# Kernel tuning notes

Hardware: AMD Instinct MI355X
Metric: run time of the kernel (lower is better)

## Reference

```python
import jax, jax.numpy as jnp
import numpy as np

B, S, MODEL_DIM = 4, 512, 128
FEAT = 2 * MODEL_DIM  # hidden feature dim must be 2*model_dim for Ws


def setup_inputs() -> dict:
    key = jax.random.key(0)
    k1, k2, k3 = jax.random.split(key, 3)
    hidden = jax.random.normal(k1, (B, S, FEAT), dtype=jnp.float32)
    # nn.Linear(2*model_dim, model_dim, bias=False): weight [model_dim, 2*model_dim]
    Ws = jax.random.normal(k2, (MODEL_DIM, FEAT), dtype=jnp.float32) * (1.0 / np.sqrt(FEAT))
    # nn.Linear(model_dim, 1, bias=False): weight [1, model_dim]
    vs = jax.random.normal(k3, (1, MODEL_DIM), dtype=jnp.float32) * (1.0 / np.sqrt(MODEL_DIM))
    return {"hidden": hidden, "Ws": Ws, "vs": vs}


def reference(hidden, Ws, vs):
    # query*key broadcast: [B, S, S, 2D]
    prod = hidden[:, None, :, :] * hidden[:, :, None, :]
    # MLP score: Linear -> tanh -> Linear, squeeze -> [B, S, S]
    h = jnp.tanh(jnp.einsum('bqkf,df->bqkd', prod, Ws))
    sjt = jnp.einsum('bqkd,d->bqk', h, vs[0])
    atten = jax.nn.softmax(sjt, axis=2)  # dropout = identity (eval)
    context = jnp.einsum('bqk,bkf->bqf', atten, hidden)
    return (context, atten)
```

## Files before the change

kernel.cpp:

```cpp
#include <hip/hip_runtime.h>
#include <hip/hip_bf16.h>

#define Bb 4
#define Ss 512
#define Ff 256
#define Dd 128

typedef __attribute__((ext_vector_type(8))) short bf8_t;
typedef __attribute__((ext_vector_type(4))) float f32x4;

__device__ __forceinline__ short bfbits(float x) {
  union { __hip_bfloat16 b; short s; } u;
  u.b = __hip_bfloat16(x);
  return u.s;
}

__device__ __forceinline__ float fast_tanh(float x) {
  float e = exp2f(x * 2.8853900818f);
  return 1.0f - 2.0f * __builtin_amdgcn_rcpf(e + 1.0f);
}

typedef __attribute__((address_space(3))) unsigned int lds_u32;
typedef const __attribute__((address_space(1))) unsigned int glb_u32;
__device__ __forceinline__ void load_lds16(const void* g, void* l) {
  __builtin_amdgcn_global_load_lds((glb_u32*)g, (lds_u32*)l, 16, 0, 0);
}

__global__ __launch_bounds__(256) void cvt_kernel(const float* __restrict__ hidden,
                                                  short* __restrict__ hbf) {
  const int idx = blockIdx.x * 256 + threadIdx.x;
  const int lin = idx * 4;
  const float4 v = *(const float4*)(hidden + lin);
  const int r = lin >> 8;
  const int c = lin & 255;
  const int cs = c ^ ((r & 7) << 3);
  short4 o = make_short4(bfbits(v.x), bfbits(v.y), bfbits(v.z), bfbits(v.w));
  *(short4*)(hbf + ((size_t)r << 8) + cs) = o;
}

__global__ __launch_bounds__(256) void score_kernel(
    const float* __restrict__ hidden, const short* __restrict__ hbf,
    const float* __restrict__ Ws, const float* __restrict__ vs,
    float* __restrict__ Sws)
{
  __shared__ __align__(16) short htile[2][32 * 256];
  __shared__ float s_full[2][512];

  const int tid   = threadIdx.x;
  const int lane  = tid & 63;
  const int w     = tid >> 6;
  const int col16 = lane & 15;
  const int grp   = lane >> 4;

  const int blk  = blockIdx.x;
  const int b    = blk & 3;
  const int pair = blk >> 2;
  const int q0   = pair * 2;
  const int c0   = q0 >> 5;

  const float* Hb  = hidden + (size_t)b * Ss * Ff;
  const short* hsb = hbf + (size_t)b * Ss * Ff;
  float*       Sb  = Sws + (size_t)b * Ss * Ss;

  bf8_t afr[2][2][8];
  #pragma unroll
  for (int ks = 0; ks < 8; ++ks) {
    const int f0 = ks * 32 + grp * 8;
    float4 h0[2], h1[2];
    #pragma unroll
    for (int g = 0; g < 2; ++g) {
      const float* hq = Hb + (size_t)(q0 + g) * Ff + f0;
      h0[g] = *(const float4*)(hq);
      h1[g] = *(const float4*)(hq + 4);
    }
    #pragma unroll
    for (int mf = 0; mf < 2; ++mf) {
      const int d = w * 32 + mf * 16 + col16;
      const float* wr = Ws + (size_t)d * Ff + f0;
      const float4 w0 = *(const float4*)(wr);
      const float4 w1 = *(const float4*)(wr + 4);
      #pragma unroll
      for (int g = 0; g < 2; ++g) {
        bf8_t t;
        t[0] = bfbits(h0[g].x * w0.x); t[1] = bfbits(h0[g].y * w0.y);
        t[2] = bfbits(h0[g].z * w0.z); t[3] = bfbits(h0[g].w * w0.w);
        t[4] = bfbits(h1[g].x * w1.x); t[5] = bfbits(h1[g].y * w1.y);
        t[6] = bfbits(h1[g].z * w1.z); t[7] = bfbits(h1[g].w * w1.w);
        afr[g][mf][ks] = t;
      }
    }
  }

  float vsv[2][4];
  #pragma unroll
  for (int mf = 0; mf < 2; ++mf)
    #pragma unroll
    for (int r = 0; r < 4; ++r)
      vsv[mf][r] = vs[w * 32 + mf * 16 + grp * 4 + r];

  {
    float* sf = (float*)s_full;
    #pragma unroll
    for (int i = 0; i < 4; ++i) sf[i * 256 + tid] = 0.f;
  }

  {
    const short* src = hsb + c0 * (32 * 256);
    #pragma unroll
    for (int i = 0; i < 4; ++i) {
      const int seg = i * 4 + w;
      load_lds16(src + seg * 512 + lane * 8, &htile[0][seg * 512]);
    }
  }

  const int swz = (col16 & 7) << 3;

  int cur = 0;
  for (int c = c0; c < 16; ++c) {
    const int k0 = c << 5;
    __syncthreads();
    if (c < 15) {
      const short* src = hsb + (c + 1) * (32 * 256);
      const int nb = cur ^ 1;
      #pragma unroll
      for (int i = 0; i < 4; ++i) {
        const int seg = i * 4 + w;
        load_lds16(src + seg * 512 + lane * 8, &htile[nb][seg * 512]);
      }
    }
    #pragma unroll
    for (int nf = 0; nf < 2; ++nf) {
      f32x4 acc[2][2] = {};
      const int rbase = nf * 4096 + col16 * 256;
      #pragma unroll
      for (int ks = 0; ks < 8; ++ks) {
        const int coff = (ks * 32 + grp * 8) ^ swz;
        const bf8_t bbv = *(const bf8_t*)(&htile[cur][rbase + coff]);
        acc[0][0] = __builtin_amdgcn_mfma_f32_16x16x32_bf16(afr[0][0][ks], bbv, acc[0][0], 0, 0, 0);
        acc[0][1] = __builtin_amdgcn_mfma_f32_16x16x32_bf16(afr[0][1][ks], bbv, acc[0][1], 0, 0, 0);
        acc[1][0] = __builtin_amdgcn_mfma_f32_16x16x32_bf16(afr[1][0][ks], bbv, acc[1][0], 0, 0, 0);
        acc[1][1] = __builtin_amdgcn_mfma_f32_16x16x32_bf16(afr[1][1][ks], bbv, acc[1][1], 0, 0, 0);
      }
      #pragma unroll
      for (int g = 0; g < 2; ++g) {
        float ps = 0.f;
        #pragma unroll
        for (int mf = 0; mf < 2; ++mf)
          #pragma unroll
          for (int r = 0; r < 4; ++r)
            ps += vsv[mf][r] * fast_tanh(acc[g][mf][r]);
        ps += __shfl_xor(ps, 16);
        ps += __shfl_xor(ps, 32);
        if (lane < 16)
          atomicAdd(&s_full[g][k0 + nf * 16 + lane], ps);
      }
    }
    cur ^= 1;
  }
  __syncthreads();

  #pragma unroll
  for (int g = 0; g < 2; ++g) {
    for (int k = q0 + tid; k < Ss; k += 256)
      Sb[(size_t)(q0 + g) * Ss + k] = s_full[g][k];
    for (int k = q0 + 2 + tid; k < Ss; k += 256)
      Sb[(size_t)k * Ss + (q0 + g)] = s_full[g][k];
  }
}

__global__ __launch_bounds__(256) void ctx_kernel(
    const float* __restrict__ hidden, const float* __restrict__ Sws,
    float* __restrict__ out)
{
  __shared__ float p[4][512];
  __shared__ float ctxp[4][4][256];

  const int tid = threadIdx.x, lane = tid & 63, w = tid >> 6;
  const int blk = blockIdx.x;
  const int b   = blk >> 7;
  const int q0  = (blk & 127) * 4;

  const float* Sb = Sws + (size_t)b * Ss * Ss;
  const float* Hb = hidden + (size_t)b * Ss * Ff;

  {
    const int q = q0 + w;
    const float* Srow = Sb + (size_t)q * Ss;
    const float4 x0 = *(const float4*)(Srow + lane * 8);
    const float4 x1 = *(const float4*)(Srow + lane * 8 + 4);
    float m = fmaxf(fmaxf(fmaxf(x0.x, x0.y), fmaxf(x0.z, x0.w)),
                    fmaxf(fmaxf(x1.x, x1.y), fmaxf(x1.z, x1.w)));
    #pragma unroll
    for (int d = 1; d < 64; d <<= 1) m = fmaxf(m, __shfl_xor(m, d));
    float4 e0, e1;
    e0.x = exp2f((x0.x - m) * 1.44269504f); e0.y = exp2f((x0.y - m) * 1.44269504f);
    e0.z = exp2f((x0.z - m) * 1.44269504f); e0.w = exp2f((x0.w - m) * 1.44269504f);
    e1.x = exp2f((x1.x - m) * 1.44269504f); e1.y = exp2f((x1.y - m) * 1.44269504f);
    e1.z = exp2f((x1.z - m) * 1.44269504f); e1.w = exp2f((x1.w - m) * 1.44269504f);
    float sm = e0.x + e0.y + e0.z + e0.w + e1.x + e1.y + e1.z + e1.w;
    #pragma unroll
    for (int d = 1; d < 64; d <<= 1) sm += __shfl_xor(sm, d);
    const float inv = 1.0f / sm;
    e0.x *= inv; e0.y *= inv; e0.z *= inv; e0.w *= inv;
    e1.x *= inv; e1.y *= inv; e1.z *= inv; e1.w *= inv;
    float* att = out + (size_t)Bb * Ss * Ff + ((size_t)(b * Ss + q)) * Ss;
    *(float4*)(att + lane * 8)     = e0;
    *(float4*)(att + lane * 8 + 4) = e1;
    *(float4*)(&p[w][lane * 8])     = e0;
    *(float4*)(&p[w][lane * 8 + 4]) = e1;
  }
  __syncthreads();

  float4 cg[4] = {{0,0,0,0},{0,0,0,0},{0,0,0,0},{0,0,0,0}};
  const float* hp = Hb + (size_t)(w * 128) * Ff + lane * 4;
  #pragma unroll 4
  for (int k = 0; k < 128; ++k) {
    const float4 h = *(const float4*)(hp + (size_t)k * Ff);
    #pragma unroll
    for (int g = 0; g < 4; ++g) {
      const float a = p[g][w * 128 + k];
      cg[g].x += a * h.x; cg[g].y += a * h.y; cg[g].z += a * h.z; cg[g].w += a * h.w;
    }
  }
  #pragma unroll
  for (int g = 0; g < 4; ++g)
    *(float4*)(&ctxp[w][g][lane * 4]) = cg[g];
  __syncthreads();
  #pragma unroll
  for (int rep = 0; rep < 4; ++rep) {
    const int idx = rep * 256 + tid;
    const int g = idx >> 8, f = idx & 255;
    out[((size_t)(b * Ss) + q0 + g) * Ff + f] =
        ctxp[0][g][f] + ctxp[1][g][f] + ctxp[2][g][f] + ctxp[3][g][f];
  }
}

__global__ __launch_bounds__(256) void selfatten_fallback(
    const float* __restrict__ hidden, const float* __restrict__ Ws,
    const float* __restrict__ vs, float* __restrict__ out)
{
  __shared__ __align__(16) short htile[2][64][264];
  __shared__ float s_part[2][4][2][64];
  __shared__ float s_full[2][512];
  __shared__ float red[8];

  const int tid = threadIdx.x, lane = tid & 63, w = tid >> 6;
  const int col16 = lane & 15, grp = lane >> 4;
  const int blk = blockIdx.x, b = blk >> 8, q0 = (blk & 255) * 2;
  const float* Hb = hidden + (size_t)b * Ss * Ff;

  bf8_t afr[2][2][8];
  #pragma unroll
  for (int ks = 0; ks < 8; ++ks) {
    const int f0 = ks * 32 + grp * 8;
    #pragma unroll
    for (int mf = 0; mf < 2; ++mf) {
      const int d = w * 32 + mf * 16 + col16;
      const float* wr = Ws + (size_t)d * Ff + f0;
      const float4 w0 = *(const float4*)(wr);
      const float4 w1 = *(const float4*)(wr + 4);
      #pragma unroll
      for (int g = 0; g < 2; ++g) {
        const float* hq = Hb + (size_t)(q0 + g) * Ff + f0;
        const float4 h0 = *(const float4*)(hq);
        const float4 h1 = *(const float4*)(hq + 4);
        bf8_t t;
        t[0] = bfbits(h0.x * w0.x); t[1] = bfbits(h0.y * w0.y);
        t[2] = bfbits(h0.z * w0.z); t[3] = bfbits(h0.w * w0.w);
        t[4] = bfbits(h1.x * w1.x); t[5] = bfbits(h1.y * w1.y);
        t[6] = bfbits(h1.z * w1.z); t[7] = bfbits(h1.w * w1.w);
        afr[g][mf][ks] = t;
      }
    }
  }
  float vsv[2][4];
  #pragma unroll
  for (int mf = 0; mf < 2; ++mf)
    #pragma unroll
    for (int r = 0; r < 4; ++r) vsv[mf][r] = vs[w * 32 + mf * 16 + grp * 4 + r];

  #pragma unroll
  for (int it = 0; it < 8; ++it) {
    const int lin = it * 2048 + tid * 8;
    const float4 v0 = *(const float4*)(Hb + lin);
    const float4 v1 = *(const float4*)(Hb + lin + 4);
    const int row = lin >> 8, col = lin & 255;
    bf8_t o;
    o[0] = bfbits(v0.x); o[1] = bfbits(v0.y); o[2] = bfbits(v0.z); o[3] = bfbits(v0.w);
    o[4] = bfbits(v1.x); o[5] = bfbits(v1.y); o[6] = bfbits(v1.z); o[7] = bfbits(v1.w);
    *(bf8_t*)(&htile[0][row][col]) = o;
  }
  __syncthreads();
  int cur = 0;
  for (int c = 0; c < 8; ++c) {
    const int k0 = c * 64, nxt = cur ^ 1, cb = c & 1;
    const float* src = Hb + (size_t)(k0 + 64) * Ff;
    #pragma unroll
    for (int nf = 0; nf < 4; ++nf) {
      float4 sv[4];
      if (c < 7) {
        #pragma unroll
        for (int i = 0; i < 2; ++i) {
          const int lin = (nf * 2 + i) * 2048 + tid * 8;
          sv[2 * i] = *(const float4*)(src + lin);
          sv[2 * i + 1] = *(const float4*)(src + lin + 4);
        }
      }
      f32x4 acc[2][2] = {};
      #pragma unroll
      for (int ks = 0; ks < 8; ++ks) {
        const bf8_t bbv = *(const bf8_t*)(&htile[cur][nf * 16 + col16][ks * 32 + grp * 8]);
        #pragma unroll
        for (int g = 0; g < 2; ++g) {
          acc[g][0] = __builtin_amdgcn_mfma_f32_16x16x32_bf16(afr[g][0][ks], bbv, acc[g][0], 0, 0, 0);
          acc[g][1] = __builtin_amdgcn_mfma_f32_16x16x32_bf16(afr[g][1][ks], bbv, acc[g][1], 0, 0, 0);
        }
      }
      #pragma unroll
      for (int g = 0; g < 2; ++g) {
        float ps = 0.f;
        #pragma unroll
        for (int mf = 0; mf < 2; ++mf)
          #pragma unroll
          for (int r = 0; r < 4; ++r) ps += vsv[mf][r] * fast_tanh(acc[g][mf][r]);
        ps += __shfl_xor(ps, 16);
        ps += __shfl_xor(ps, 32);
        if (lane < 16) s_part[cb][w][g][nf * 16 + lane] = ps;
      }
      if (c < 7) {
        #pragma unroll
        for (int i = 0; i < 2; ++i) {
          const int lin = (nf * 2 + i) * 2048 + tid * 8;
          const int row = lin >> 8, col = lin & 255;
          const float4 a = sv[2 * i], bsv = sv[2 * i + 1];
          bf8_t o;
          o[0] = bfbits(a.x); o[1] = bfbits(a.y); o[2] = bfbits(a.z); o[3] = bfbits(a.w);
          o[4] = bfbits(bsv.x); o[5] = bfbits(bsv.y); o[6] = bfbits(bsv.z); o[7] = bfbits(bsv.w);
          *(bf8_t*)(&htile[nxt][row][col]) = o;
        }
      }
    }
    __syncthreads();
    if (tid < 128) {
      const int g = tid >> 6, key = tid & 63;
      s_full[g][k0 + key] = s_part[cb][0][g][key] + s_part[cb][1][g][key] +
                            s_part[cb][2][g][key] + s_part[cb][3][g][key];
    }
    cur = nxt;
  }
  __syncthreads();
  float av[2][2];
  #pragma unroll
  for (int g = 0; g < 2; ++g) {
    const float s0 = s_full[g][tid], s1 = s_full[g][tid + 256];
    float m = fmaxf(s0, s1);
    #pragma unroll
    for (int d = 1; d < 64; d <<= 1) m = fmaxf(m, __shfl_xor(m, d));
    if (lane == 0) red[w] = m;
    __syncthreads();
    m = fmaxf(fmaxf(red[0], red[1]), fmaxf(red[2], red[3]));
    const float p0 = exp2f((s0 - m) * 1.44269504f);
    const float p1 = exp2f((s1 - m) * 1.44269504f);
    float sm = p0 + p1;
    #pragma unroll
    for (int d = 1; d < 64; d <<= 1) sm += __shfl_xor(sm, d);
    if (lane == 0) red[4 + w] = sm;
    __syncthreads();
    const float inv = 1.0f / (red[4] + red[5] + red[6] + red[7]);
    av[g][0] = p0 * inv; av[g][1] = p1 * inv;
    float* attp = out + (size_t)Bb * Ss * Ff + ((size_t)(b * Ss + q0 + g)) * Ss;
    attp[tid] = av[g][0];
    attp[tid + 256] = av[g][1];
    __syncthreads();
  }
  s_full[0][tid] = av[0][0]; s_full[0][tid + 256] = av[0][1];
  s_full[1][tid] = av[1][0]; s_full[1][tid + 256] = av[1][1];
  __syncthreads();
  float* ctxp = (float*)htile;
  float4 c0v = {0,0,0,0}, c1v = {0,0,0,0};
  const float* hp = Hb + (size_t)(w * 128) * Ff + lane * 4;
  #pragma unroll 8
  for (int k = 0; k < 128; ++k) {
    const float4 h = *(const float4*)(hp + (size_t)k * Ff);
    const float a0 = s_full[0][w * 128 + k];
    const float a1 = s_full[1][w * 128 + k];
    c0v.x += a0 * h.x; c0v.y += a0 * h.y; c0v.z += a0 * h.z; c0v.w += a0 * h.w;
    c1v.x += a1 * h.x; c1v.y += a1 * h.y; c1v.z += a1 * h.z; c1v.w += a1 * h.w;
  }
  *(float4*)(&ctxp[(w * 2 + 0) * 256 + lane * 4]) = c0v;
  *(float4*)(&ctxp[(w * 2 + 1) * 256 + lane * 4]) = c1v;
  __syncthreads();
  #pragma unroll
  for (int rep = 0; rep < 2; ++rep) {
    const int idx = tid + rep * 256;
    const int g = idx >> 8, f = idx & 255;
    out[((size_t)(b * Ss) + q0 + g) * Ff + f] =
        ctxp[(0 * 2 + g) * 256 + f] + ctxp[(1 * 2 + g) * 256 + f] +
        ctxp[(2 * 2 + g) * 256 + f] + ctxp[(3 * 2 + g) * 256 + f];
  }
}

extern "C" void kernel_launch(void* const* d_in, const int* in_sizes, int n_in,
                              void* d_out, int out_size, void* d_ws, size_t ws_size,
                              hipStream_t stream) {
  (void)in_sizes; (void)n_in; (void)out_size;
  const float* hidden = (const float*)d_in[0];
  const float* Ws     = (const float*)d_in[1];
  const float* vs     = (const float*)d_in[2];
  float* out          = (float*)d_out;

  const size_t hbf_bytes = (size_t)Bb * Ss * Ff * sizeof(short);
  const size_t sws_bytes = (size_t)Bb * Ss * Ss * sizeof(float);
  if (ws_size >= hbf_bytes + sws_bytes) {
    short* hbf = (short*)d_ws;
    float* Sws = (float*)((char*)d_ws + hbf_bytes);
    cvt_kernel<<<dim3(Bb * Ss * Ff / 4 / 256), dim3(256), 0, stream>>>(hidden, hbf);
    score_kernel<<<dim3(Bb * Ss / 2), dim3(256), 0, stream>>>(hidden, hbf, Ws, vs, Sws);
    ctx_kernel<<<dim3(Bb * Ss / 4), dim3(256), 0, stream>>>(hidden, Sws, out);
  } else {
    selfatten_fallback<<<dim3(Bb * Ss / 2), dim3(256), 0, stream>>>(hidden, Ws, vs, out);
  }
}
```

Measured before the change: 87.82 us.

## Split score kernel over eight waves with 64-key tiles

The score kernel now runs 512 threads (8 waves), each wave owning 16 of the 128 projection dims instead of 32. This halves the per-wave A-fragment registers and the MFMA work per wave. The key tile loaded into LDS grows to 64 rows, which halves the number of loop iterations and barriers. In exchange, LDS use doubles to about 64KB per block, which may limit how many blocks fit per CU, and eight waves now do atomic adds into the same shared score rows.

```diff
diff --git a/kernel.cpp b/kernel.cpp
--- a/kernel.cpp
+++ b/kernel.cpp
@@ -38,12 +38,12 @@
   *(short4*)(hbf + ((size_t)r << 8) + cs) = o;
 }
 
-__global__ __launch_bounds__(256) void score_kernel(
+__global__ __launch_bounds__(512, 4) void score_kernel(
     const float* __restrict__ hidden, const short* __restrict__ hbf,
     const float* __restrict__ Ws, const float* __restrict__ vs,
     float* __restrict__ Sws)
 {
-  __shared__ __align__(16) short htile[2][32 * 256];
+  __shared__ __align__(16) short htile[2][64 * 256];
   __shared__ float s_full[2][512];
 
   const int tid   = threadIdx.x;
@@ -56,59 +56,50 @@
   const int b    = blk & 3;
   const int pair = blk >> 2;
   const int q0   = pair * 2;
-  const int c0   = q0 >> 5;
+  const int c0   = q0 >> 6;
 
   const float* Hb  = hidden + (size_t)b * Ss * Ff;
   const short* hsb = hbf + (size_t)b * Ss * Ff;
   float*       Sb  = Sws + (size_t)b * Ss * Ss;
 
-  bf8_t afr[2][2][8];
-  #pragma unroll
-  for (int ks = 0; ks < 8; ++ks) {
-    const int f0 = ks * 32 + grp * 8;
-    float4 h0[2], h1[2];
-    #pragma unroll
-    for (int g = 0; g < 2; ++g) {
-      const float* hq = Hb + (size_t)(q0 + g) * Ff + f0;
-      h0[g] = *(const float4*)(hq);
-      h1[g] = *(const float4*)(hq + 4);
-    }
-    #pragma unroll
-    for (int mf = 0; mf < 2; ++mf) {
-      const int d = w * 32 + mf * 16 + col16;
-      const float* wr = Ws + (size_t)d * Ff + f0;
-      const float4 w0 = *(const float4*)(wr);
-      const float4 w1 = *(const float4*)(wr + 4);
+  bf8_t afr[2][8];
+  {
+    const int d = w * 16 + col16;
+    const float* wr0 = Ws + (size_t)d * Ff;
+    #pragma unroll
+    for (int ks = 0; ks < 8; ++ks) {
+      const int f0 = ks * 32 + grp * 8;
+      const float4 w0 = *(const float4*)(wr0 + f0);
+      const float4 w1 = *(const float4*)(wr0 + f0 + 4);
       #pragma unroll
       for (int g = 0; g < 2; ++g) {
+        const float* hq = Hb + (size_t)(q0 + g) * Ff + f0;
+        const float4 h0 = *(const float4*)(hq);
+        const float4 h1 = *(const float4*)(hq + 4);
         bf8_t t;
-        t[0] = bfbits(h0[g].x * w0.x); t[1] = bfbits(h0[g].y * w0.y);
-        t[2] = bfbits(h0[g].z * w0.z); t[3] = bfbits(h0[g].w * w0.w);
-        t[4] = bfbits(h1[g].x * w1.x); t[5] = bfbits(h1[g].y * w1.y);
-        t[6] = bfbits(h1[g].z * w1.z); t[7] = bfbits(h1[g].w * w1.w);
-        afr[g][mf][ks] = t;
-      }
-    }
-  }
-
-  float vsv[2][4];
-  #pragma unroll
-  for (int mf = 0; mf < 2; ++mf)
-    #pragma unroll
-    for (int r = 0; r < 4; ++r)
-      vsv[mf][r] = vs[w * 32 + mf * 16 + grp * 4 + r];
+        t[0] = bfbits(h0.x * w0.x); t[1] = bfbits(h0.y * w0.y);
+        t[2] = bfbits(h0.z * w0.z); t[3] = bfbits(h0.w * w0.w);
+        t[4] = bfbits(h1.x * w1.x); t[5] = bfbits(h1.y * w1.y);
+        t[6] = bfbits(h1.z * w1.z); t[7] = bfbits(h1.w * w1.w);
+        afr[g][ks] = t;
+      }
+    }
+  }
+
+  float vsv[4];
+  #pragma unroll
+  for (int r = 0; r < 4; ++r) vsv[r] = vs[w * 16 + grp * 4 + r];
 
   {
     float* sf = (float*)s_full;
-    #pragma unroll
-    for (int i = 0; i < 4; ++i) sf[i * 256 + tid] = 0.f;
+    sf[tid] = 0.f; sf[tid + 512] = 0.f;
   }
 
   {
-    const short* src = hsb + c0 * (32 * 256);
+    const short* src = hsb + c0 * (64 * 256);
     #pragma unroll
     for (int i = 0; i < 4; ++i) {
-      const int seg = i * 4 + w;
+      const int seg = i * 8 + w;
       load_lds16(src + seg * 512 + lane * 8, &htile[0][seg * 512]);
     }
   }
@@ -116,39 +107,35 @@
   const int swz = (col16 & 7) << 3;
 
   int cur = 0;
-  for (int c = c0; c < 16; ++c) {
-    const int k0 = c << 5;
+  for (int c = c0; c < 8; ++c) {
+    const int k0 = c << 6;
     __syncthreads();
-    if (c < 15) {
-      const short* src = hsb + (c + 1) * (32 * 256);
+    if (c < 7) {
+      const short* src = hsb + (c + 1) * (64 * 256);
       const int nb = cur ^ 1;
       #pragma unroll
       for (int i = 0; i < 4; ++i) {
-        const int seg = i * 4 + w;
+        const int seg = i * 8 + w;
         load_lds16(src + seg * 512 + lane * 8, &htile[nb][seg * 512]);
       }
     }
     #pragma unroll
-    for (int nf = 0; nf < 2; ++nf) {
-      f32x4 acc[2][2] = {};
+    for (int nf = 0; nf < 4; ++nf) {
+      f32x4 acc[2] = {};
       const int rbase = nf * 4096 + col16 * 256;
       #pragma unroll
       for (int ks = 0; ks < 8; ++ks) {
         const int coff = (ks * 32 + grp * 8) ^ swz;
         const bf8_t bbv = *(const bf8_t*)(&htile[cur][rbase + coff]);
-        acc[0][0] = __builtin_amdgcn_mfma_f32_16x16x32_bf16(afr[0][0][ks], bbv, acc[0][0], 0, 0, 0);
-        acc[0][1] = __builtin_amdgcn_mfma_f32_16x16x32_bf16(afr[0][1][ks], bbv, acc[0][1], 0, 0, 0);
-        acc[1][0] = __builtin_amdgcn_mfma_f32_16x16x32_bf16(afr[1][0][ks], bbv, acc[1][0], 0, 0, 0);
-        acc[1][1] = __builtin_amdgcn_mfma_f32_16x16x32_bf16(afr[1][1][ks], bbv, acc[1][1], 0, 0, 0);
+        acc[0] = __builtin_amdgcn_mfma_f32_16x16x32_bf16(afr[0][ks], bbv, acc[0], 0, 0, 0);
+        acc[1] = __builtin_amdgcn_mfma_f32_16x16x32_bf16(afr[1][ks], bbv, acc[1], 0, 0, 0);
       }
       #pragma unroll
       for (int g = 0; g < 2; ++g) {
         float ps = 0.f;
         #pragma unroll
-        for (int mf = 0; mf < 2; ++mf)
-          #pragma unroll
-          for (int r = 0; r < 4; ++r)
-            ps += vsv[mf][r] * fast_tanh(acc[g][mf][r]);
+        for (int r = 0; r < 4; ++r)
+          ps += vsv[r] * fast_tanh(acc[g][r]);
         ps += __shfl_xor(ps, 16);
         ps += __shfl_xor(ps, 32);
         if (lane < 16)
@@ -161,9 +148,9 @@
 
   #pragma unroll
   for (int g = 0; g < 2; ++g) {
-    for (int k = q0 + tid; k < Ss; k += 256)
+    for (int k = q0 + tid; k < Ss; k += 512)
       Sb[(size_t)(q0 + g) * Ss + k] = s_full[g][k];
-    for (int k = q0 + 2 + tid; k < Ss; k += 256)
+    for (int k = q0 + 2 + tid; k < Ss; k += 512)
       Sb[(size_t)k * Ss + (q0 + g)] = s_full[g][k];
   }
 }
@@ -415,7 +402,7 @@
     short* hbf = (short*)d_ws;
     float* Sws = (float*)((char*)d_ws + hbf_bytes);
     cvt_kernel<<<dim3(Bb * Ss * Ff / 4 / 256), dim3(256), 0, stream>>>(hidden, hbf);
-    score_kernel<<<dim3(Bb * Ss / 2), dim3(256), 0, stream>>>(hidden, hbf, Ws, vs, Sws);
+    score_kernel<<<dim3(Bb * Ss / 2), dim3(512), 0, stream>>>(hidden, hbf, Ws, vs, Sws);
     ctx_kernel<<<dim3(Bb * Ss / 4), dim3(256), 0, stream>>>(hidden, Sws, out);
   } else {
     selfatten_fallback<<<dim3(Bb * Ss / 2), dim3(256), 0, stream>>>(hidden, Ws, vs, out);
```

Measured after the change: 106.6 us. +21.3%, slower.

## Load score B-fragments directly from global into registers, dropping LDS staging

Applied to the files above, without the earlier changes.

The score kernel no longer stages bf16 key tiles in double-buffered LDS through global_load_lds. Each lane now reads its MFMA B fragments straight from global memory, prefetching the next 16-key block into registers, and the triangular start is tightened to 16-key granularity. The tanh/vs reduction is rewritten algebraically as sum(v) - 2*sum(v/(e+1)), the transposed scores are written as float2 pairs, and the cvt kernel writes unswizzled 8-element vectors. This removes LDS traffic and block-wide barriers, at the cost of more global/L2 loads and more register pressure.

```diff
diff --git a/kernel.cpp b/kernel.cpp
--- a/kernel.cpp
+++ b/kernel.cpp
@@ -20,22 +20,16 @@
   return 1.0f - 2.0f * __builtin_amdgcn_rcpf(e + 1.0f);
 }
 
-typedef __attribute__((address_space(3))) unsigned int lds_u32;
-typedef const __attribute__((address_space(1))) unsigned int glb_u32;
-__device__ __forceinline__ void load_lds16(const void* g, void* l) {
-  __builtin_amdgcn_global_load_lds((glb_u32*)g, (lds_u32*)l, 16, 0, 0);
-}
-
 __global__ __launch_bounds__(256) void cvt_kernel(const float* __restrict__ hidden,
                                                   short* __restrict__ hbf) {
   const int idx = blockIdx.x * 256 + threadIdx.x;
-  const int lin = idx * 4;
-  const float4 v = *(const float4*)(hidden + lin);
-  const int r = lin >> 8;
-  const int c = lin & 255;
-  const int cs = c ^ ((r & 7) << 3);
-  short4 o = make_short4(bfbits(v.x), bfbits(v.y), bfbits(v.z), bfbits(v.w));
-  *(short4*)(hbf + ((size_t)r << 8) + cs) = o;
+  const size_t lin = (size_t)idx * 8;
+  const float4 v0 = *(const float4*)(hidden + lin);
+  const float4 v1 = *(const float4*)(hidden + lin + 4);
+  bf8_t o;
+  o[0] = bfbits(v0.x); o[1] = bfbits(v0.y); o[2] = bfbits(v0.z); o[3] = bfbits(v0.w);
+  o[4] = bfbits(v1.x); o[5] = bfbits(v1.y); o[6] = bfbits(v1.z); o[7] = bfbits(v1.w);
+  *(bf8_t*)(hbf + lin) = o;
 }
 
 __global__ __launch_bounds__(256) void score_kernel(
@@ -43,7 +37,6 @@
     const float* __restrict__ Ws, const float* __restrict__ vs,
     float* __restrict__ Sws)
 {
-  __shared__ __align__(16) short htile[2][32 * 256];
   __shared__ float s_full[2][512];
 
   const int tid   = threadIdx.x;
@@ -56,7 +49,7 @@
   const int b    = blk & 3;
   const int pair = blk >> 2;
   const int q0   = pair * 2;
-  const int c0   = q0 >> 5;
+  const int kstart = q0 & ~15;
 
   const float* Hb  = hidden + (size_t)b * Ss * Ff;
   const short* hsb = hbf + (size_t)b * Ss * Ff;
@@ -91,80 +84,73 @@
     }
   }
 
-  float vsv[2][4];
+  float m2v[2][4];
+  float base = 0.f;
   #pragma unroll
   for (int mf = 0; mf < 2; ++mf)
     #pragma unroll
-    for (int r = 0; r < 4; ++r)
-      vsv[mf][r] = vs[w * 32 + mf * 16 + grp * 4 + r];
+    for (int r = 0; r < 4; ++r) {
+      const float v = vs[w * 32 + mf * 16 + grp * 4 + r];
+      m2v[mf][r] = -2.0f * v;
+      base += v;
+    }
 
   {
     float* sf = (float*)s_full;
-    #pragma unroll
-    for (int i = 0; i < 4; ++i) sf[i * 256 + tid] = 0.f;
-  }
-
-  {
-    const short* src = hsb + c0 * (32 * 256);
-    #pragma unroll
-    for (int i = 0; i < 4; ++i) {
-      const int seg = i * 4 + w;
-      load_lds16(src + seg * 512 + lane * 8, &htile[0][seg * 512]);
-    }
-  }
-
-  const int swz = (col16 & 7) << 3;
-
-  int cur = 0;
-  for (int c = c0; c < 16; ++c) {
-    const int k0 = c << 5;
-    __syncthreads();
-    if (c < 15) {
-      const short* src = hsb + (c + 1) * (32 * 256);
-      const int nb = cur ^ 1;
-      #pragma unroll
-      for (int i = 0; i < 4; ++i) {
-        const int seg = i * 4 + w;
-        load_lds16(src + seg * 512 + lane * 8, &htile[nb][seg * 512]);
-      }
-    }
-    #pragma unroll
-    for (int nf = 0; nf < 2; ++nf) {
-      f32x4 acc[2][2] = {};
-      const int rbase = nf * 4096 + col16 * 256;
-      #pragma unroll
-      for (int ks = 0; ks < 8; ++ks) {
-        const int coff = (ks * 32 + grp * 8) ^ swz;
-        const bf8_t bbv = *(const bf8_t*)(&htile[cur][rbase + coff]);
-        acc[0][0] = __builtin_amdgcn_mfma_f32_16x16x32_bf16(afr[0][0][ks], bbv, acc[0][0], 0, 0, 0);
-        acc[0][1] = __builtin_amdgcn_mfma_f32_16x16x32_bf16(afr[0][1][ks], bbv, acc[0][1], 0, 0, 0);
-        acc[1][0] = __builtin_amdgcn_mfma_f32_16x16x32_bf16(afr[1][0][ks], bbv, acc[1][0], 0, 0, 0);
-        acc[1][1] = __builtin_amdgcn_mfma_f32_16x16x32_bf16(afr[1][1][ks], bbv, acc[1][1], 0, 0, 0);
-      }
-      #pragma unroll
-      for (int g = 0; g < 2; ++g) {
-        float ps = 0.f;
+    sf[tid] = 0.f; sf[tid + 256] = 0.f; sf[tid + 512] = 0.f; sf[tid + 768] = 0.f;
+  }
+  __syncthreads();
+
+  const short* lanep = hsb + (size_t)(kstart + col16) * 256 + grp * 8;
+  const int nkf = (Ss - kstart) >> 4;
+
+  bf8_t bA[8];
+  #pragma unroll
+  for (int ks = 0; ks < 8; ++ks) bA[ks] = *(const bf8_t*)(lanep + ks * 32);
+
+  for (int i = 0; i < nkf; ++i) {
+    const int k16 = kstart + i * 16;
+    bf8_t bB[8];
+    if (i + 1 < nkf) {
+      const short* np = lanep + (size_t)(i + 1) * (16 * 256);
+      #pragma unroll
+      for (int ks = 0; ks < 8; ++ks) bB[ks] = *(const bf8_t*)(np + ks * 32);
+    }
+    f32x4 acc[2][2] = {};
+    #pragma unroll
+    for (int ks = 0; ks < 8; ++ks) {
+      acc[0][0] = __builtin_amdgcn_mfma_f32_16x16x32_bf16(afr[0][0][ks], bA[ks], acc[0][0], 0, 0, 0);
+      acc[0][1] = __builtin_amdgcn_mfma_f32_16x16x32_bf16(afr[0][1][ks], bA[ks], acc[0][1], 0, 0, 0);
+      acc[1][0] = __builtin_amdgcn_mfma_f32_16x16x32_bf16(afr[1][0][ks], bA[ks], acc[1][0], 0, 0, 0);
+      acc[1][1] = __builtin_amdgcn_mfma_f32_16x16x32_bf16(afr[1][1][ks], bA[ks], acc[1][1], 0, 0, 0);
+    }
+    #pragma unroll
+    for (int g = 0; g < 2; ++g) {
+      float ps = base;
+      #pragma unroll
+      for (int mf = 0; mf < 2; ++mf)
         #pragma unroll
-        for (int mf = 0; mf < 2; ++mf)
-          #pragma unroll
-          for (int r = 0; r < 4; ++r)
-            ps += vsv[mf][r] * fast_tanh(acc[g][mf][r]);
-        ps += __shfl_xor(ps, 16);
-        ps += __shfl_xor(ps, 32);
-        if (lane < 16)
-          atomicAdd(&s_full[g][k0 + nf * 16 + lane], ps);
-      }
-    }
-    cur ^= 1;
-  }
-  __syncthreads();
-
-  #pragma unroll
-  for (int g = 0; g < 2; ++g) {
-    for (int k = q0 + tid; k < Ss; k += 256)
-      Sb[(size_t)(q0 + g) * Ss + k] = s_full[g][k];
-    for (int k = q0 + 2 + tid; k < Ss; k += 256)
-      Sb[(size_t)k * Ss + (q0 + g)] = s_full[g][k];
+        for (int r = 0; r < 4; ++r) {
+          const float e = exp2f(acc[g][mf][r] * 2.8853900818f);
+          ps += m2v[mf][r] * __builtin_amdgcn_rcpf(e + 1.0f);
+        }
+      ps += __shfl_xor(ps, 16);
+      ps += __shfl_xor(ps, 32);
+      if (lane < 16)
+        atomicAdd(&s_full[g][k16 + lane], ps);
+    }
+    #pragma unroll
+    for (int ks = 0; ks < 8; ++ks) bA[ks] = bB[ks];
+  }
+  __syncthreads();
+
+  for (int k = q0 + tid; k < Ss; k += 256)
+    Sb[(size_t)q0 * Ss + k] = s_full[0][k];
+  for (int k = q0 + tid; k < Ss; k += 256)
+    Sb[(size_t)(q0 + 1) * Ss + k] = s_full[1][k];
+  for (int k = q0 + 2 + tid; k < Ss; k += 256) {
+    const float2 v = make_float2(s_full[0][k], s_full[1][k]);
+    *(float2*)(&Sb[(size_t)k * Ss + q0]) = v;
   }
 }
 
@@ -414,7 +400,7 @@
   if (ws_size >= hbf_bytes + sws_bytes) {
     short* hbf = (short*)d_ws;
     float* Sws = (float*)((char*)d_ws + hbf_bytes);
-    cvt_kernel<<<dim3(Bb * Ss * Ff / 4 / 256), dim3(256), 0, stream>>>(hidden, hbf);
+    cvt_kernel<<<dim3(Bb * Ss * Ff / 8 / 256), dim3(256), 0, stream>>>(hidden, hbf);
     score_kernel<<<dim3(Bb * Ss / 2), dim3(256), 0, stream>>>(hidden, hbf, Ws, vs, Sws);
     ctx_kernel<<<dim3(Bb * Ss / 4), dim3(256), 0, stream>>>(hidden, Sws, out);
   } else {
```

After: 106.0 us. +20.8%, slower.
